# Kernel optimization log

Measured on AMD Instinct MI355X. Metric: run time of the kernel, lower is better.

Reference implementation:

```python
import jax, jax.numpy as jnp
import numpy as np

B, S, E, H = 4, 2048, 1024, 16
D = E // H  # head_dim


def setup_inputs() -> dict:
    key = jax.random.key(0)
    ks = jax.random.split(key, 5)
    scale = 1.0 / np.sqrt(E)
    return {
        "qkv": jax.random.normal(ks[0], (B, S, E), jnp.float32),
        "in_w": jax.random.normal(ks[1], (3 * E, E), jnp.float32) * scale,
        "in_b": jax.random.normal(ks[2], (3 * E,), jnp.float32) * scale,
        "out_w": jax.random.normal(ks[3], (E, E), jnp.float32) * scale,
        "out_b": jax.random.normal(ks[4], (E,), jnp.float32) * scale,
    }


def reference(qkv, in_w, in_b, out_w, out_b):
    # in_proj: torch Linear -> x @ W^T + b, output [B,S,3E]
    x1 = jnp.einsum('bse,fe->bsf', qkv, in_w) + in_b
    q, k, v = jnp.split(x1, 3, axis=2)  # each [B,S,E]
    # reshape to heads: [B,H,S,D] (contiguous head_dim slices == reshape)
    q = q.reshape(B, S, H, D).transpose(0, 2, 1, 3)
    k = k.reshape(B, S, H, D).transpose(0, 2, 1, 3)
    v = v.reshape(B, S, H, D).transpose(0, 2, 1, 3)
    scores = jnp.einsum('bhqd,bhkd->bhqk', q, k) / jnp.sqrt(jnp.float32(D))
    attn = jax.nn.softmax(scores, axis=-1)  # dropout p=0.0 -> identity
    out = jnp.einsum('bhqk,bhkd->bhqd', attn, v)  # [B,H,S,D]
    out = out.transpose(0, 2, 1, 3).reshape(B, S, E)
    return jnp.einsum('bse,fe->bsf', out, out_w) + out_b
```

## Files before the change

kernel.cpp:

```cpp
#include <hip/hip_runtime.h>


typedef __attribute__((ext_vector_type(8))) short s16x8;
typedef __attribute__((ext_vector_type(8))) __bf16 bf16x8;
typedef __attribute__((ext_vector_type(4))) float f32x4;
typedef __attribute__((ext_vector_type(16))) float f32x16;
typedef __attribute__((ext_vector_type(4))) unsigned short u16x4;
typedef __attribute__((ext_vector_type(4))) unsigned int u32x4;

#define QSCALE_F 0.18033688011112042f

#if __has_builtin(__builtin_amdgcn_exp2f)
#define EXP2F(x) __builtin_amdgcn_exp2f(x)
#else
#define EXP2F(x) exp2f(x)
#endif

__device__ __forceinline__ unsigned short f2bf(float f) {
  unsigned int u = __builtin_bit_cast(unsigned int, f);
  u += 0x7fffu + ((u >> 16) & 1u);
  return (unsigned short)(u >> 16);
}

__device__ __forceinline__ f32x4 mfma16(s16x8 a, s16x8 b, f32x4 c) {
  return __builtin_amdgcn_mfma_f32_16x16x32_bf16(
      __builtin_bit_cast(bf16x8, a), __builtin_bit_cast(bf16x8, b), c, 0, 0, 0);
}
__device__ __forceinline__ f32x16 mfma32(s16x8 a, s16x8 b, f32x16 c) {
  return __builtin_amdgcn_mfma_f32_32x32x16_bf16(
      __builtin_bit_cast(bf16x8, a), __builtin_bit_cast(bf16x8, b), c, 0, 0, 0);
}

__device__ __forceinline__ unsigned cvtpk(float lo, float hi) {
  unsigned r;
  asm("v_cvt_pk_bf16_f32 %0, %1, %2" : "=v"(r) : "v"(lo), "v"(hi));
  return r;
}
__device__ __forceinline__ void p32swap(unsigned &a, unsigned &b) {
  asm volatile("v_permlane32_swap_b32 %0, %1" : "+v"(a), "+v"(b));
}

#define GLL16(gp, lp) __builtin_amdgcn_global_load_lds(                       \
    (const __attribute__((address_space(1))) void*)(gp),                      \
    (__attribute__((address_space(3))) void*)(lp), 16, 0, 0)

__global__ void cvt_f32_bf16(const float* __restrict__ in,
                             unsigned short* __restrict__ out,
                             int n, int scale_n) {
  int idx = (blockIdx.x * 256 + threadIdx.x) * 4;
  int stride = gridDim.x * 256 * 4;
  for (int i = idx; i < n; i += stride) {
    const float4 v = *reinterpret_cast<const float4*>(in + i);
    const float sc = (i < scale_n) ? QSCALE_F : 1.0f;
    u16x4 r;
    r.x = f2bf(v.x * sc); r.y = f2bf(v.y * sc);
    r.z = f2bf(v.z * sc); r.w = f2bf(v.w * sc);
    *reinterpret_cast<u16x4*>(out + i) = r;
  }
}

template <bool OUT_BF16>
__global__ __launch_bounds__(256, 2) void gemm_nt(
    const unsigned short* __restrict__ A, const unsigned short* __restrict__ B,
    const float* __restrict__ bias, void* __restrict__ Cout,
    int M, int N, int K, int qscale_cols) {
  __shared__ __align__(16) unsigned short As[128 * 64];
  __shared__ __align__(16) unsigned short Bs[128 * 64];
  const int tid = threadIdx.x;
  const int lane = tid & 63, w = tid >> 6;
  const int l15 = lane & 15, l4 = lane >> 4;
  const int wr = w >> 1, wc = w & 1;
  const int bm = blockIdx.y * 128, bn = blockIdx.x * 128;

  f32x4 acc[4][4];
#pragma unroll
  for (int i = 0; i < 4; ++i)
#pragma unroll
    for (int j = 0; j < 4; ++j) acc[i][j] = (f32x4){0.f, 0.f, 0.f, 0.f};

  for (int kt = 0; kt < K; kt += 64) {
#pragma unroll
    for (int j = 0; j < 4; ++j) {
      const int gb = (j * 4 + w) * 64;
      const int g = gb + lane;
      const int row = g >> 3, seg = g & 7;
      GLL16(A + (size_t)(bm + row) * K + kt + seg * 8, As + gb * 8);
      GLL16(B + (size_t)(bn + row) * K + kt + seg * 8, Bs + gb * 8);
    }
    __syncthreads();
#pragma unroll
    for (int kk = 0; kk < 2; ++kk) {
      s16x8 a[4], b[4];
#pragma unroll
      for (int mi = 0; mi < 4; ++mi)
        a[mi] = *reinterpret_cast<const s16x8*>(
            As + (wr * 64 + mi * 16 + l15) * 64 + kk * 32 + l4 * 8);
#pragma unroll
      for (int ni = 0; ni < 4; ++ni)
        b[ni] = *reinterpret_cast<const s16x8*>(
            Bs + (wc * 64 + ni * 16 + l15) * 64 + kk * 32 + l4 * 8);
#pragma unroll
      for (int mi = 0; mi < 4; ++mi)
#pragma unroll
        for (int ni = 0; ni < 4; ++ni)
          acc[mi][ni] = mfma16(a[mi], b[ni], acc[mi][ni]);
    }
    __syncthreads();
  }
#pragma unroll
  for (int mi = 0; mi < 4; ++mi) {
#pragma unroll
    for (int ni = 0; ni < 4; ++ni) {
      const int col = bn + wc * 64 + ni * 16 + l15;
      const float bsc = (col < qscale_cols) ? QSCALE_F : 1.0f;
      const float bv = bias[col] * bsc;
#pragma unroll
      for (int r = 0; r < 4; ++r) {
        const int row = bm + wr * 64 + mi * 16 + l4 * 4 + r;
        const float val = acc[mi][ni][r] + bv;
        if (OUT_BF16)
          ((unsigned short*)Cout)[(size_t)row * N + col] = f2bf(val);
        else
          ((float*)Cout)[(size_t)row * N + col] = val;
      }
    }
  }
}

__global__ __launch_bounds__(256, 4) void attn_fwd(
    const unsigned short* __restrict__ X1, unsigned short* __restrict__ O) {
  __shared__ __align__(16) unsigned short Ks[2][64 * 64];
  __shared__ __align__(16) unsigned short Vt[2][64 * 64];

  const int id = blockIdx.x;
  const int xc = id & 7, r0 = id >> 3;
  const int bh = xc * 8 + (r0 & 7);
  const int qt = r0 >> 3;
  const int b = bh >> 4, h = bh & 15;
  const int tid = threadIdx.x;
  const int lane = tid & 63, w = tid >> 6;
  const int l31 = lane & 31, hi = lane >> 5;

  const unsigned short* Qp = X1 + (size_t)b * 2048 * 3072 + h * 64;
  const unsigned short* Kp = Qp + 1024;
  const unsigned short* Vp = Qp + 2048;
  const int q0 = qt * 128 + w * 32;

  s16x8 qf[4];
#pragma unroll
  for (int kk = 0; kk < 4; ++kk)
    qf[kk] = *reinterpret_cast<const s16x8*>(
        Qp + (size_t)(q0 + l31) * 3072 + kk * 16 + hi * 8);

  f32x16 oacc[2];
#pragma unroll
  for (int db = 0; db < 2; ++db)
#pragma unroll
    for (int i = 0; i < 16; ++i) oacc[db][i] = 0.f;
  float m_r = -1e30f, l_r = 0.f;

  const int vchunk0 = (w) * 1024, vchunk1 = (w + 4) * 1024;
#define STAGE_K(kt_, buf_)                                                    \
  {                                                                           \
    _Pragma("unroll") for (int j = 0; j < 2; ++j) {                           \
      const int chunk = (j * 4 + w) * 1024;                                   \
      const int o = chunk + lane * 16;                                        \
      const int row = o >> 7;                                                 \
      const int srcb = (o & 127) ^ ((row & 7) << 4);                          \
      GLL16(Kp + (size_t)((kt_) + row) * 3072 + (srcb >> 1),                  \
            (char*)Ks[buf_] + chunk);                                         \
    }                                                                         \
  }
#define LOAD_V(kt_, vr_)                                                      \
  {                                                                           \
    _Pragma("unroll") for (int j = 0; j < 2; ++j) {                           \
      const int seg = w + 4 * j;                                              \
      vr_[j] = *reinterpret_cast<const s16x8*>(                               \
          Vp + (size_t)((kt_) + lane) * 3072 + seg * 8);                      \
    }                                                                         \
  }
#define WRITE_V(vr_, buf_)                                                    \
  {                                                                           \
    _Pragma("unroll") for (int j = 0; j < 2; ++j) {                           \
      const int seg = w + 4 * j;                                              \
      _Pragma("unroll") for (int e = 0; e < 8; ++e) {                         \
        const int d = seg * 8 + e;                                            \
        const int byt = d * 128 + ((lane * 2) ^ (e << 4));                    \
        *(unsigned short*)((char*)Vt[buf_] + byt) = (unsigned short)vr_[j][e];\
      }                                                                       \
    }                                                                         \
  }

  s16x8 vnxt[2];
  LOAD_V(0, vnxt);
  STAGE_K(0, 0);
  WRITE_V(vnxt, 0);
  __syncthreads();

  for (int t = 0; t < 32; ++t) {
    const int cur = t & 1;
    const unsigned short* Ksc = Ks[cur];
    const unsigned short* Vtc = Vt[cur];
    if (t < 31) {
      LOAD_V((t + 1) * 64, vnxt);
      STAGE_K((t + 1) * 64, cur ^ 1);
    }

    f32x16 sa[2];
#pragma unroll
    for (int sub = 0; sub < 2; ++sub)
#pragma unroll
      for (int i = 0; i < 16; ++i) sa[sub][i] = 0.f;
    __builtin_amdgcn_s_setprio(1);
#pragma unroll
    for (int sub = 0; sub < 2; ++sub) {
      const int row = sub * 32 + l31;
#pragma unroll
      for (int kk = 0; kk < 4; ++kk) {
        const int byt = row * 128 + ((kk * 32 + hi * 16) ^ ((l31 & 7) << 4));
        s16x8 ka = *reinterpret_cast<const s16x8*>((const char*)Ksc + byt);
        sa[sub] = mfma32(ka, qf[kk], sa[sub]);
      }
    }
    __builtin_amdgcn_s_setprio(0);

    float m0 = sa[0][0], m1 = sa[0][1], m2 = sa[0][2], m3 = sa[0][3];
#pragma unroll
    for (int i = 4; i < 16; i += 4) {
      m0 = fmaxf(m0, sa[0][i]);     m1 = fmaxf(m1, sa[0][i + 1]);
      m2 = fmaxf(m2, sa[0][i + 2]); m3 = fmaxf(m3, sa[0][i + 3]);
    }
#pragma unroll
    for (int i = 0; i < 16; i += 4) {
      m0 = fmaxf(m0, sa[1][i]);     m1 = fmaxf(m1, sa[1][i + 1]);
      m2 = fmaxf(m2, sa[1][i + 2]); m3 = fmaxf(m3, sa[1][i + 3]);
    }
    float mx = fmaxf(fmaxf(m0, m1), fmaxf(m2, m3));
    mx = fmaxf(mx, __shfl_xor(mx, 32));

    if (__any(mx > m_r + 8.0f)) {
      const float mnew = fmaxf(m_r, mx);
      const float alpha = EXP2F(m_r - mnew);
      m_r = mnew;
      l_r *= alpha;
#pragma unroll
      for (int r = 0; r < 16; ++r) {
        const float ar = __shfl(alpha, (r & 3) + 8 * (r >> 2) + 4 * hi);
        oacc[0][r] *= ar;
        oacc[1][r] *= ar;
      }
    }

    float s0 = 0.f, s1 = 0.f, s2 = 0.f, s3 = 0.f;
#pragma unroll
    for (int sub = 0; sub < 2; ++sub)
#pragma unroll
      for (int i = 0; i < 16; i += 4) {
        sa[sub][i]     = EXP2F(sa[sub][i] - m_r);     s0 += sa[sub][i];
        sa[sub][i + 1] = EXP2F(sa[sub][i + 1] - m_r); s1 += sa[sub][i + 1];
        sa[sub][i + 2] = EXP2F(sa[sub][i + 2] - m_r); s2 += sa[sub][i + 2];
        sa[sub][i + 3] = EXP2F(sa[sub][i + 3] - m_r); s3 += sa[sub][i + 3];
      }
    float rsum = (s0 + s1) + (s2 + s3);
    rsum += __shfl_xor(rsum, 32);
    l_r += rsum;

    s16x8 pa[2][2];
#pragma unroll
    for (int sub = 0; sub < 2; ++sub)
#pragma unroll
      for (int g = 0; g < 2; ++g) {
        unsigned c0 = cvtpk(sa[sub][g * 8 + 0], sa[sub][g * 8 + 1]);
        unsigned c1 = cvtpk(sa[sub][g * 8 + 2], sa[sub][g * 8 + 3]);
        unsigned c2 = cvtpk(sa[sub][g * 8 + 4], sa[sub][g * 8 + 5]);
        unsigned c3 = cvtpk(sa[sub][g * 8 + 6], sa[sub][g * 8 + 7]);
        p32swap(c0, c2);
        p32swap(c1, c3);
        u32x4 tt = {c0, c1, c2, c3};
        pa[sub][g] = __builtin_bit_cast(s16x8, tt);
      }

    __builtin_amdgcn_s_setprio(1);
#pragma unroll
    for (int db = 0; db < 2; ++db) {
      const int row = db * 32 + l31;
#pragma unroll
      for (int sub = 0; sub < 2; ++sub)
#pragma unroll
        for (int g = 0; g < 2; ++g) {
          const int byt =
              row * 128 + (((sub * 2 + g) * 32 + hi * 16) ^ ((l31 & 7) << 4));
          s16x8 vb = *reinterpret_cast<const s16x8*>((const char*)Vtc + byt);
          oacc[db] = mfma32(pa[sub][g], vb, oacc[db]);
        }
    }
    __builtin_amdgcn_s_setprio(0);

    if (t < 31) WRITE_V(vnxt, cur ^ 1);
    __syncthreads();
  }

  const float invl = 1.0f / l_r;
#pragma unroll
  for (int r = 0; r < 16; ++r) {
    const int crow = (r & 3) + 8 * (r >> 2) + 4 * hi;
    const float ir = __shfl(invl, crow);
    const size_t base = (size_t)(b * 2048 + q0 + crow) * 1024 + h * 64 + l31;
    O[base] = f2bf(oacc[0][r] * ir);
    O[base + 32] = f2bf(oacc[1][r] * ir);
  }
}

extern "C" void kernel_launch(void* const* d_in, const int* in_sizes, int n_in,
                              void* d_out, int out_size, void* d_ws,
                              size_t ws_size, hipStream_t stream) {
  const float* qkv   = (const float*)d_in[0];
  const float* in_w  = (const float*)d_in[1];
  const float* in_b  = (const float*)d_in[2];
  const float* out_w = (const float*)d_in[3];
  const float* out_b = (const float*)d_in[4];
  float* out = (float*)d_out;
  char* ws = (char*)d_ws;

  unsigned short* qkv_bf  = (unsigned short*)(ws);
  unsigned short* win_bf  = (unsigned short*)(ws + 16777216);
  unsigned short* wout_bf = (unsigned short*)(ws + 23068672);
  unsigned short* x1      = (unsigned short*)(ws + 25165824);
  unsigned short* attn_out = qkv_bf;

  cvt_f32_bf16<<<2048, 256, 0, stream>>>(qkv, qkv_bf, 8388608, 0);
  cvt_f32_bf16<<<1024, 256, 0, stream>>>(in_w, win_bf, 3145728, 1048576);
  cvt_f32_bf16<<<512, 256, 0, stream>>>(out_w, wout_bf, 1048576, 0);

  gemm_nt<true><<<dim3(24, 64), 256, 0, stream>>>(
      qkv_bf, win_bf, in_b, (void*)x1, 8192, 3072, 1024, 1024);

  attn_fwd<<<1024, 256, 0, stream>>>(x1, attn_out);

  gemm_nt<false><<<dim3(8, 64), 256, 0, stream>>>(
      attn_out, wout_bf, out_b, (void*)out, 8192, 1024, 1024, 0);
}
```

Before: 206.8 us.

## Replace input-projection GEMM with 8-phase pipelined 128x256 tile kernel

```diff
diff --git a/kernel.cpp b/kernel.cpp
--- a/kernel.cpp
+++ b/kernel.cpp
@@ -43,6 +43,14 @@
 #define GLL16(gp, lp) __builtin_amdgcn_global_load_lds(                       \
     (const __attribute__((address_space(1))) void*)(gp),                      \
     (__attribute__((address_space(3))) void*)(lp), 16, 0, 0)
+
+#define SBAR0 __builtin_amdgcn_sched_barrier(0)
+#define HWBAR __builtin_amdgcn_s_barrier()
+#define LGKM0 asm volatile("s_waitcnt lgkmcnt(0)" ::: "memory")
+#define VMC3 asm volatile("s_waitcnt vmcnt(3)" ::: "memory")
+#define VMC0 asm volatile("s_waitcnt vmcnt(0)" ::: "memory")
+#define PRIO1 __builtin_amdgcn_s_setprio(1)
+#define PRIO0 __builtin_amdgcn_s_setprio(0)
 
 __global__ void cvt_f32_bf16(const float* __restrict__ in,
                              unsigned short* __restrict__ out,
@@ -59,6 +67,139 @@
   }
 }
 
+__global__ __launch_bounds__(512, 2) void gemm1_8ph(
+    const unsigned short* __restrict__ A, const unsigned short* __restrict__ B,
+    const float* __restrict__ bias, unsigned short* __restrict__ C,
+    int M, int N, int K, int qscale_cols) {
+  __shared__ __align__(16) unsigned short As[2][128 * 64];
+  __shared__ __align__(16) unsigned short Bs[2][256 * 64];
+  const int tid = threadIdx.x;
+  const int lane = tid & 63, w = tid >> 6;
+  const int l15 = lane & 15, l4 = (lane >> 4) & 3;
+  const int wm = w >> 2, wn = w & 3;
+  const int lane16 = lane * 16;
+  const int swz = (l15 & 7) << 4;
+  const int bm = blockIdx.y * 128, bn = blockIdx.x * 256;
+  const int NIT = K >> 7;
+
+#define STG_A(buf_, h_, kt_) {                                                \
+    const int parel = (h_) * 8192 + w * 1024;                                 \
+    const int o = parel + lane16;                                             \
+    const int row = o >> 7;                                                   \
+    const int cb = (o & 127) ^ ((row & 7) << 4);                              \
+    GLL16(A + (size_t)(bm + row) * K + (kt_) * 64 + (cb >> 1),                \
+          (char*)As[buf_] + parel);                                           \
+  }
+#define STG_B(buf_, h_, kt_) {                                                \
+    _Pragma("unroll") for (int j = 0; j < 2; ++j) {                           \
+      const int parel = (h_) * 16384 + (j * 8 + w) * 1024;                    \
+      const int o = parel + lane16;                                           \
+      const int row = o >> 7;                                                 \
+      const int cb = (o & 127) ^ ((row & 7) << 4);                            \
+      GLL16(B + (size_t)(bn + row) * K + (kt_) * 64 + (cb >> 1),              \
+            (char*)Bs[buf_] + parel);                                         \
+    }                                                                         \
+  }
+#define RD_A(buf_, qm_, dst_) {                                               \
+    _Pragma("unroll") for (int mt = 0; mt < 2; ++mt)                          \
+      _Pragma("unroll") for (int kk = 0; kk < 2; ++kk)                        \
+        dst_[mt][kk] = *(const s16x8*)((const char*)As[buf_] +                \
+            (wm * 64 + (qm_) * 32 + mt * 16 + l15) * 128 +                    \
+            ((kk * 64 + l4 * 16) ^ swz));                                     \
+  }
+#define RD_B(buf_, qn_, dst_) {                                               \
+    _Pragma("unroll") for (int nt = 0; nt < 2; ++nt)                          \
+      _Pragma("unroll") for (int kk = 0; kk < 2; ++kk)                        \
+        dst_[nt][kk] = *(const s16x8*)((const char*)Bs[buf_] +                \
+            (wn * 64 + (qn_) * 32 + nt * 16 + l15) * 128 +                    \
+            ((kk * 64 + l4 * 16) ^ swz));                                     \
+  }
+#define MM8(qm_, qn_, a_, b_) {                                               \
+    _Pragma("unroll") for (int mt = 0; mt < 2; ++mt)                          \
+      _Pragma("unroll") for (int nt = 0; nt < 2; ++nt)                        \
+        _Pragma("unroll") for (int kk = 0; kk < 2; ++kk)                      \
+          acc[(qm_) * 2 + mt][(qn_) * 2 + nt] = mfma16(                       \
+              a_[mt][kk], b_[nt][kk], acc[(qm_) * 2 + mt][(qn_) * 2 + nt]);   \
+  }
+
+  f32x4 acc[4][4];
+#pragma unroll
+  for (int i = 0; i < 4; ++i)
+#pragma unroll
+    for (int j = 0; j < 4; ++j) acc[i][j] = (f32x4){0.f, 0.f, 0.f, 0.f};
+
+  STG_B(0, 0, 0); STG_A(0, 0, 0); STG_A(0, 1, 0); STG_B(0, 1, 0);
+  STG_B(1, 0, 1); STG_A(1, 0, 1);
+  VMC3;
+  SBAR0; HWBAR;
+
+  s16x8 a[2][2], b0[2][2], b1[2][2];
+  for (int i = 0; i < NIT; ++i) {
+    const bool st = (i < NIT - 1);
+    STG_A(1, 1, 2 * i + 1);
+    RD_A(0, 0, a); RD_B(0, 0, b0);
+    SBAR0; HWBAR; LGKM0; SBAR0;
+    PRIO1; MM8(0, 0, a, b0); PRIO0;
+    SBAR0; HWBAR;
+    STG_B(1, 1, 2 * i + 1);
+    RD_B(0, 1, b1);
+    SBAR0; HWBAR; LGKM0; SBAR0;
+    PRIO1; MM8(0, 1, a, b1); PRIO0;
+    SBAR0; HWBAR;
+    if (st) STG_B(0, 0, 2 * i + 2);
+    RD_A(0, 1, a);
+    SBAR0; HWBAR; LGKM0; SBAR0;
+    PRIO1; MM8(1, 1, a, b1); PRIO0;
+    SBAR0; HWBAR;
+    if (st) STG_A(0, 0, 2 * i + 2);
+    SBAR0; HWBAR;
+    PRIO1; MM8(1, 0, a, b0); PRIO0;
+    SBAR0;
+    if (st) { VMC3; } else { VMC0; }
+    HWBAR;
+    if (st) STG_A(0, 1, 2 * i + 2);
+    RD_A(1, 0, a); RD_B(1, 0, b0);
+    SBAR0; HWBAR; LGKM0; SBAR0;
+    PRIO1; MM8(0, 0, a, b0); PRIO0;
+    SBAR0; HWBAR;
+    if (st) STG_B(0, 1, 2 * i + 2);
+    RD_B(1, 1, b1);
+    SBAR0; HWBAR; LGKM0; SBAR0;
+    PRIO1; MM8(0, 1, a, b1); PRIO0;
+    SBAR0; HWBAR;
+    if (st) STG_B(1, 0, 2 * i + 3);
+    RD_A(1, 1, a);
+    SBAR0; HWBAR; LGKM0; SBAR0;
+    PRIO1; MM8(1, 1, a, b1); PRIO0;
+    SBAR0; HWBAR;
+    if (st) STG_A(1, 0, 2 * i + 3);
+    SBAR0; HWBAR;
+    PRIO1; MM8(1, 0, a, b0); PRIO0;
+    SBAR0;
+    if (st) VMC3;
+    HWBAR;
+  }
+
+#pragma unroll
+  for (int mi = 0; mi < 4; ++mi)
+#pragma unroll
+    for (int ni = 0; ni < 4; ++ni) {
+      const int col = bn + wn * 64 + ni * 16 + l15;
+      const float bsc = (col < qscale_cols) ? QSCALE_F : 1.0f;
+      const float bv = bias[col] * bsc;
+#pragma unroll
+      for (int r = 0; r < 4; ++r) {
+        const int row = bm + wm * 64 + mi * 16 + l4 * 4 + r;
+        C[(size_t)row * N + col] = f2bf(acc[mi][ni][r] + bv);
+      }
+    }
+#undef STG_A
+#undef STG_B
+#undef RD_A
+#undef RD_B
+#undef MM8
+}
+
 template <bool OUT_BF16>
 __global__ __launch_bounds__(256, 2) void gemm_nt(
     const unsigned short* __restrict__ A, const unsigned short* __restrict__ B,
@@ -159,7 +300,6 @@
     for (int i = 0; i < 16; ++i) oacc[db][i] = 0.f;
   float m_r = -1e30f, l_r = 0.f;
 
-  const int vchunk0 = (w) * 1024, vchunk1 = (w + 4) * 1024;
 #define STAGE_K(kt_, buf_)                                                    \
   {                                                                           \
     _Pragma("unroll") for (int j = 0; j < 2; ++j) {                           \
@@ -211,7 +351,7 @@
     for (int sub = 0; sub < 2; ++sub)
 #pragma unroll
       for (int i = 0; i < 16; ++i) sa[sub][i] = 0.f;
-    __builtin_amdgcn_s_setprio(1);
+    PRIO1;
 #pragma unroll
     for (int sub = 0; sub < 2; ++sub) {
       const int row = sub * 32 + l31;
@@ -222,7 +362,7 @@
         sa[sub] = mfma32(ka, qf[kk], sa[sub]);
       }
     }
-    __builtin_amdgcn_s_setprio(0);
+    PRIO0;
 
     float m0 = sa[0][0], m1 = sa[0][1], m2 = sa[0][2], m3 = sa[0][3];
 #pragma unroll
@@ -280,7 +420,7 @@
         pa[sub][g] = __builtin_bit_cast(s16x8, tt);
       }
 
-    __builtin_amdgcn_s_setprio(1);
+    PRIO1;
 #pragma unroll
     for (int db = 0; db < 2; ++db) {
       const int row = db * 32 + l31;
@@ -294,7 +434,7 @@
           oacc[db] = mfma32(pa[sub][g], vb, oacc[db]);
         }
     }
-    __builtin_amdgcn_s_setprio(0);
+    PRIO0;
 
     if (t < 31) WRITE_V(vnxt, cur ^ 1);
     __syncthreads();
@@ -332,8 +472,8 @@
   cvt_f32_bf16<<<1024, 256, 0, stream>>>(in_w, win_bf, 3145728, 1048576);
   cvt_f32_bf16<<<512, 256, 0, stream>>>(out_w, wout_bf, 1048576, 0);
 
-  gemm_nt<true><<<dim3(24, 64), 256, 0, stream>>>(
-      qkv_bf, win_bf, in_b, (void*)x1, 8192, 3072, 1024, 1024);
+  gemm1_8ph<<<dim3(12, 64), 512, 0, stream>>>(
+      qkv_bf, win_bf, in_b, x1, 8192, 3072, 1024, 1024);
 
   attn_fwd<<<1024, 256, 0, stream>>>(x1, attn_out);
 
```

After: 217.2 us. 1.05x slower.

## Replace QKV projection GEMM with 256x256 tile eight-phase pipelined kernel

Applied to the files above, without the earlier changes.

```diff
diff --git a/kernel.cpp b/kernel.cpp
--- a/kernel.cpp
+++ b/kernel.cpp
@@ -43,6 +43,14 @@
 #define GLL16(gp, lp) __builtin_amdgcn_global_load_lds(                       \
     (const __attribute__((address_space(1))) void*)(gp),                      \
     (__attribute__((address_space(3))) void*)(lp), 16, 0, 0)
+
+#define SBAR0 __builtin_amdgcn_sched_barrier(0)
+#define HWBAR __builtin_amdgcn_s_barrier()
+#define LGKM0 asm volatile("s_waitcnt lgkmcnt(0)" ::: "memory")
+#define VMC4 asm volatile("s_waitcnt vmcnt(4)" ::: "memory")
+#define VMC0 asm volatile("s_waitcnt vmcnt(0)" ::: "memory")
+#define PRIO1 __builtin_amdgcn_s_setprio(1)
+#define PRIO0 __builtin_amdgcn_s_setprio(0)
 
 __global__ void cvt_f32_bf16(const float* __restrict__ in,
                              unsigned short* __restrict__ out,
@@ -59,6 +67,121 @@
   }
 }
 
+__global__ __launch_bounds__(512, 2) void gemm1_8ph(
+    const unsigned short* __restrict__ A, const unsigned short* __restrict__ B,
+    const float* __restrict__ bias, unsigned short* __restrict__ C,
+    int M, int N, int K, int qscale_cols) {
+  __shared__ __align__(16) unsigned short As[2][256 * 64];
+  __shared__ __align__(16) unsigned short Bs[2][256 * 64];
+  const int NT = K >> 6;
+  const int id = blockIdx.x;
+  const int mi_ = (id & 7) * 4 + ((id >> 3) & 3);
+  const int ni_ = id >> 5;
+  const int bm = mi_ * 256, bn = ni_ * 256;
+
+  const int tid = threadIdx.x;
+  const int lane = tid & 63, w = tid >> 6;
+  const int l15 = lane & 15, l4 = (lane >> 4) & 3;
+  const int wm = w >> 2, wn = w & 3;
+  const int swz = (l15 & 7) << 4;
+
+#define STG_HALF(ldsc_, gb_, ktel_) {                                         \
+    _Pragma("unroll") for (int s_ = 0; s_ < 2; ++s_) {                        \
+      const int o = (w * 2 + s_) * 1024 + lane * 16;                          \
+      const int row_ = o >> 7;                                                \
+      const int cb_ = (o & 127) ^ ((row_ & 7) << 4);                          \
+      GLL16((gb_) + (size_t)row_ * K + (ktel_) + (cb_ >> 1),                  \
+            (char*)(ldsc_) + o);                                              \
+    }                                                                         \
+  }
+#define RD_A(buf_, qm_, dst_) {                                               \
+    _Pragma("unroll") for (int mt = 0; mt < 4; ++mt)                          \
+      _Pragma("unroll") for (int kk = 0; kk < 2; ++kk)                        \
+        dst_[mt][kk] = *(const s16x8*)((const char*)As[buf_] +                \
+            (wm * 128 + (qm_) * 64 + mt * 16 + l15) * 128 +                   \
+            ((kk * 64 + l4 * 16) ^ swz));                                     \
+  }
+#define RD_B(buf_, qn_, dst_) {                                               \
+    _Pragma("unroll") for (int nt = 0; nt < 2; ++nt)                          \
+      _Pragma("unroll") for (int kk = 0; kk < 2; ++kk)                        \
+        dst_[nt][kk] = *(const s16x8*)((const char*)Bs[buf_] +                \
+            (wn * 64 + (qn_) * 32 + nt * 16 + l15) * 128 +                    \
+            ((kk * 64 + l4 * 16) ^ swz));                                     \
+  }
+#define MMQ(qm_, qn_, a_, b_) {                                               \
+    _Pragma("unroll") for (int mt = 0; mt < 4; ++mt)                          \
+      _Pragma("unroll") for (int nt = 0; nt < 2; ++nt)                        \
+        _Pragma("unroll") for (int kk = 0; kk < 2; ++kk)                      \
+          acc[(qm_) * 4 + mt][(qn_) * 2 + nt] = mfma16(                       \
+              a_[mt][kk], b_[nt][kk], acc[(qm_) * 4 + mt][(qn_) * 2 + nt]);   \
+  }
+
+  f32x4 acc[8][4];
+#pragma unroll
+  for (int i = 0; i < 8; ++i)
+#pragma unroll
+    for (int j = 0; j < 4; ++j) acc[i][j] = (f32x4){0.f, 0.f, 0.f, 0.f};
+
+  const unsigned short* Ah0 = A + (size_t)bm * K;
+  const unsigned short* Ah1 = A + (size_t)(bm + 128) * K;
+  const unsigned short* Bh0 = B + (size_t)bn * K;
+  const unsigned short* Bh1 = B + (size_t)(bn + 128) * K;
+
+  STG_HALF(Bs[0], Bh0, 0);
+  STG_HALF(As[0], Ah0, 0);
+  STG_HALF((char*)Bs[0] + 16384, Bh1, 0);
+  STG_HALF((char*)As[0] + 16384, Ah1, 0);
+  STG_HALF(Bs[1], Bh0, 64);
+  STG_HALF(As[1], Ah0, 64);
+  VMC4;
+  SBAR0; HWBAR;
+
+  s16x8 a[4][2], b0[2][2], b1[2][2];
+  for (int t = 0; t < NT; ++t) {
+    const int cur = t & 1, oth = cur ^ 1;
+    RD_A(cur, 0, a);
+    RD_B(cur, 0, b0);
+    if (t + 1 < NT) STG_HALF((char*)Bs[oth] + 16384, Bh1, (t + 1) * 64);
+    SBAR0; HWBAR; LGKM0; SBAR0;
+    PRIO1; MMQ(0, 0, a, b0); PRIO0;
+    SBAR0; HWBAR;
+    RD_B(cur, 1, b1);
+    if (t + 1 < NT) STG_HALF((char*)As[oth] + 16384, Ah1, (t + 1) * 64);
+    SBAR0; HWBAR; LGKM0; SBAR0;
+    PRIO1; MMQ(0, 1, a, b1); PRIO0;
+    SBAR0; HWBAR;
+    RD_A(cur, 1, a);
+    if (t + 2 < NT) STG_HALF(Bs[cur], Bh0, (t + 2) * 64);
+    SBAR0; HWBAR; LGKM0; SBAR0;
+    PRIO1; MMQ(1, 1, a, b1); PRIO0;
+    SBAR0; HWBAR;
+    if (t + 2 < NT) STG_HALF(As[cur], Ah0, (t + 2) * 64);
+    SBAR0; HWBAR;
+    PRIO1; MMQ(1, 0, a, b0); PRIO0;
+    SBAR0;
+    if (t + 2 < NT) { VMC4; } else { VMC0; }
+    HWBAR;
+  }
+
+#pragma unroll
+  for (int mi = 0; mi < 8; ++mi)
+#pragma unroll
+    for (int ni = 0; ni < 4; ++ni) {
+      const int col = bn + wn * 64 + ni * 16 + l15;
+      const float bsc = (col < qscale_cols) ? QSCALE_F : 1.0f;
+      const float bv = bias[col] * bsc;
+#pragma unroll
+      for (int r = 0; r < 4; ++r) {
+        const int row = bm + wm * 128 + mi * 16 + l4 * 4 + r;
+        C[(size_t)row * N + col] = f2bf(acc[mi][ni][r] + bv);
+      }
+    }
+#undef STG_HALF
+#undef RD_A
+#undef RD_B
+#undef MMQ
+}
+
 template <bool OUT_BF16>
 __global__ __launch_bounds__(256, 2) void gemm_nt(
     const unsigned short* __restrict__ A, const unsigned short* __restrict__ B,
@@ -159,7 +282,6 @@
     for (int i = 0; i < 16; ++i) oacc[db][i] = 0.f;
   float m_r = -1e30f, l_r = 0.f;
 
-  const int vchunk0 = (w) * 1024, vchunk1 = (w + 4) * 1024;
 #define STAGE_K(kt_, buf_)                                                    \
   {                                                                           \
     _Pragma("unroll") for (int j = 0; j < 2; ++j) {                           \
@@ -211,7 +333,7 @@
     for (int sub = 0; sub < 2; ++sub)
 #pragma unroll
       for (int i = 0; i < 16; ++i) sa[sub][i] = 0.f;
-    __builtin_amdgcn_s_setprio(1);
+    PRIO1;
 #pragma unroll
     for (int sub = 0; sub < 2; ++sub) {
       const int row = sub * 32 + l31;
@@ -222,7 +344,7 @@
         sa[sub] = mfma32(ka, qf[kk], sa[sub]);
       }
     }
-    __builtin_amdgcn_s_setprio(0);
+    PRIO0;
 
     float m0 = sa[0][0], m1 = sa[0][1], m2 = sa[0][2], m3 = sa[0][3];
 #pragma unroll
@@ -280,7 +402,7 @@
         pa[sub][g] = __builtin_bit_cast(s16x8, tt);
       }
 
-    __builtin_amdgcn_s_setprio(1);
+    PRIO1;
 #pragma unroll
     for (int db = 0; db < 2; ++db) {
       const int row = db * 32 + l31;
@@ -294,7 +416,7 @@
           oacc[db] = mfma32(pa[sub][g], vb, oacc[db]);
         }
     }
-    __builtin_amdgcn_s_setprio(0);
+    PRIO0;
 
     if (t < 31) WRITE_V(vnxt, cur ^ 1);
     __syncthreads();
@@ -332,8 +454,8 @@
   cvt_f32_bf16<<<1024, 256, 0, stream>>>(in_w, win_bf, 3145728, 1048576);
   cvt_f32_bf16<<<512, 256, 0, stream>>>(out_w, wout_bf, 1048576, 0);
 
-  gemm_nt<true><<<dim3(24, 64), 256, 0, stream>>>(
-      qkv_bf, win_bf, in_b, (void*)x1, 8192, 3072, 1024, 1024);
+  gemm1_8ph<<<384, 512, 0, stream>>>(
+      qkv_bf, win_bf, in_b, x1, 8192, 3072, 1024, 1024);
 
   attn_fwd<<<1024, 256, 0, stream>>>(x1, attn_out);
 
```

Result: no change. 208.8 us (+1.0%).
